# Kernel optimization log

Hardware: AMD Instinct MI355X
Metric: run time of the kernel (lower is better)

The kernel has to match this reference:

```python
import jax, jax.numpy as jnp
import numpy as np

DIM = 1024
HEADS = 16
HEAD_DIM = 64
INNER = HEADS * HEAD_DIM
SCALE = HEAD_DIM ** -0.5


def setup_inputs() -> dict:
    key = jax.random.key(0)
    k1, k2, k3, k4 = jax.random.split(key, 4)
    x = jax.random.normal(k1, (4, 2048, DIM), dtype=jnp.float32)
    # nn.Linear(dim, 3*inner) without bias; weight stored [out, in], we keep [in, out]
    w_qkv = jax.random.normal(k2, (DIM, 3 * INNER), dtype=jnp.float32) * (DIM ** -0.5)
    w_proj = jax.random.normal(k3, (INNER, DIM), dtype=jnp.float32) * (INNER ** -0.5)
    b_proj = jax.random.normal(k4, (DIM,), dtype=jnp.float32) * 0.01
    return {"x": x, "w_qkv": w_qkv, "w_proj": w_proj, "b_proj": b_proj}


def reference(x, w_qkv, w_proj, b_proj):
    B, N, _ = x.shape
    qkv = x @ w_qkv                                   # [B,N,3*inner]
    qkv = qkv.reshape(B, N, 3, HEADS, HEAD_DIM)
    q = qkv[:, :, 0].transpose(0, 2, 1, 3)           # [B,H,N,D]
    k = qkv[:, :, 1].transpose(0, 2, 1, 3)
    v = qkv[:, :, 2].transpose(0, 2, 1, 3)
    attn = jnp.einsum("bhqd,bhkd->bhqk", q, k) * SCALE
    attn = jax.nn.softmax(attn, axis=-1)
    out = jnp.einsum("bhqk,bhkd->bhqd", attn, v)     # [B,H,N,D]
    out = out.transpose(0, 2, 1, 3).reshape(B, N, INNER)
    return out @ w_proj + b_proj
```

## Files before the change

kernel.cpp:

```cpp
#include <hip/hip_runtime.h>

typedef unsigned short u16;
typedef unsigned int   u32;
typedef __attribute__((ext_vector_type(2))) float    f32x2;
typedef __attribute__((ext_vector_type(4))) float    f32x4;
typedef __attribute__((ext_vector_type(8))) __bf16   bf16x8;
typedef __attribute__((ext_vector_type(8))) unsigned short u16x8;
typedef __attribute__((ext_vector_type(4))) unsigned short u16x4;
typedef __attribute__((ext_vector_type(4))) float    float4v;

#define MFMA16(a,b,c) __builtin_amdgcn_mfma_f32_16x16x32_bf16((a),(b),(c),0,0,0)
#define QSCALE 0.18033688011112042f

__device__ __forceinline__ u16 f2b(float f){
  union { float f; unsigned u; } v; v.f = f;
  return (u16)((v.u + 0x7fffu + ((v.u >> 16) & 1u)) >> 16);
}

__device__ __forceinline__ u32 cvt_pk_bf16(float lo, float hi){
  u32 r;
  asm("v_cvt_pk_bf16_f32 %0, %1, %2" : "=v"(r) : "v"(lo), "v"(hi));
  return r;
}

__device__ __forceinline__ float exp2_raw(float x){
  float r;
  asm("v_exp_f32 %0, %1" : "=v"(r) : "v"(x));
  return r;
}

__device__ __forceinline__ f32x2 lo2(f32x4 v){ return __builtin_shufflevector(v, v, 0, 1); }
__device__ __forceinline__ f32x2 hi2(f32x4 v){ return __builtin_shufflevector(v, v, 2, 3); }

__device__ __forceinline__ void gload_lds16(const void* g, void* l){
  __builtin_amdgcn_global_load_lds(
      (const __attribute__((address_space(1))) void*)g,
      (__attribute__((address_space(3))) void*)l, 16, 0, 0);
}

__global__ void cast_f32_bf16(const float* __restrict__ in, u16* __restrict__ out, int n4){
  int i = blockIdx.x * blockDim.x + threadIdx.x;
  int st = gridDim.x * blockDim.x;
  for (; i < n4; i += st){
    float4v v = ((const float4v*)in)[i];
    u16x4 o;
    o[0] = f2b(v[0]); o[1] = f2b(v[1]); o[2] = f2b(v[2]); o[3] = f2b(v[3]);
    ((u16x4*)out)[i] = o;
  }
}

__global__ void tcast(const float* __restrict__ src, u16* __restrict__ dst, int R, int C){
  __shared__ float tile[32][33];
  int tx = threadIdx.x, ty = threadIdx.y;
  int c0 = blockIdx.x * 32, r0 = blockIdx.y * 32;
  #pragma unroll
  for (int i = 0; i < 4; i++)
    tile[ty + i*8][tx] = src[(long)(r0 + ty + i*8) * C + c0 + tx];
  __syncthreads();
  #pragma unroll
  for (int i = 0; i < 4; i++)
    dst[(long)(c0 + ty + i*8) * R + r0 + tx] = f2b(tile[tx][ty + i*8]);
}

template<int MODE>
__global__ __launch_bounds__(512, 2) void gemm8(
    const u16* __restrict__ A, const u16* __restrict__ Bt,
    int M, int N, int K,
    float* __restrict__ outF, const float* __restrict__ bias,
    u16* __restrict__ qb, u16* __restrict__ kb, u16* __restrict__ vtb)
{
  extern __shared__ u16 lds[];
  u16* aL = lds;
  u16* bL = lds + 49152;

  const int t  = threadIdx.x;
  const int l  = t & 63, lr = l & 15, lg = l >> 4;
  const int w  = t >> 6;
  const int wm = w >> 2, wn = (w >> 1) & 1, wk = w & 1;
  const int bid = blockIdx.x;
  const int xcd = bid & 7, idx = bid >> 3;
  const long mbase = (long)(xcd*4 + (idx & 3)) * 256;
  const long nbase = (long)(idx >> 2) * 128;

  const int xr0 = t >> 3;
  const int xc  = t & 7;
  const int xswz = (xc ^ (xr0 & 7)) << 3;

#define STG(F_) do { \
    const int T_ = (F_) >> 2, h_ = (F_) & 3, slot_ = T_ % 3; \
    if ((h_ & 1) == 0){ const int ah = h_ >> 1; \
      const u16* g_ = A + (mbase + ah*128 + xr0)*(long)K + T_*64 + xswz; \
      u16* d_ = aL + slot_*16384 + ah*8192 + t*8; \
      gload_lds16(g_, d_); \
      gload_lds16(g_ + 64*(long)K, d_ + 4096); \
    } else { const int bh_ = h_ >> 1; \
      const u16* g_ = Bt + (nbase + bh_*64 + xr0)*(long)K + T_*64 + xswz; \
      gload_lds16(g_, bL + slot_*8192 + bh_*4096 + t*8); } \
  } while(0)

#define VMCNT(n) asm volatile("s_waitcnt vmcnt(" #n ")" ::: "memory")
#define BAR() __builtin_amdgcn_s_barrier()

  f32x4 z = {0.f,0.f,0.f,0.f};
  f32x4 acc[8][4];
  #pragma unroll
  for (int a = 0; a < 8; a++)
    #pragma unroll
    for (int j = 0; j < 4; j++) acc[a][j] = z;

  const int kc = wk*4;

  STG(0); STG(1); STG(2); STG(3);
  STG(4); STG(5); STG(6); STG(7);
  VMCNT(6);
  BAR();

  for (int T = 0; T < 16; ++T){
    const int abuf = (T % 3) * 16384;
    const int bbuf = (T % 3) * 8192;
    bf16x8 afi[8], bfj[4];

    #pragma unroll
    for (int j = 0; j < 4; j++){
      const int rb = wn*64 + j*16 + lr;
      bfj[j] = *(const bf16x8*)&bL[bbuf + rb*64 + (((kc+lg)^(rb&7))<<3)];
    }
    #pragma unroll
    for (int i = 0; i < 8; i++){
      const int ra = wm*128 + i*16 + lr;
      afi[i] = *(const bf16x8*)&aL[abuf + ra*64 + (((kc+lg)^(ra&7))<<3)];
    }
    if (T < 14){
      STG(4*(T+2)); STG(4*(T+2)+1); STG(4*(T+2)+2); STG(4*(T+2)+3);
      VMCNT(6);
    } else if (T == 14){
      VMCNT(0);
    }
    BAR();
    __builtin_amdgcn_s_setprio(1);
    #pragma unroll
    for (int i = 0; i < 8; i++)
      #pragma unroll
      for (int j = 0; j < 4; j++)
        acc[i][j] = MFMA16(afi[i], bfj[j], acc[i][j]);
    __builtin_amdgcn_s_setprio(0);
    BAR();
  }
#undef STG
#undef VMCNT
#undef BAR

  if (wk){
    #pragma unroll
    for (int a = 0; a < 8; a++){
      f32x4 t0 = acc[a][0]; acc[a][0] = acc[a][2]; acc[a][2] = t0;
      f32x4 t1 = acc[a][1]; acc[a][1] = acc[a][3]; acc[a][3] = t1;
    }
  }
  f32x4* red = (f32x4*)lds;
  const int pb = (wm*2 + wn)*2;
  const int wme = pb + (1 - wk);
  const int rme = pb + wk;
  #pragma unroll
  for (int a = 0; a < 8; a++){
    red[(wme*2 + 0)*64 + l] = acc[a][2];
    red[(wme*2 + 1)*64 + l] = acc[a][3];
    __builtin_amdgcn_s_barrier();
    acc[a][0] += red[(rme*2 + 0)*64 + l];
    acc[a][1] += red[(rme*2 + 1)*64 + l];
    __builtin_amdgcn_s_barrier();
  }

  if (MODE == 0){
    #pragma unroll
    for (int a = 0; a < 8; a++){
      #pragma unroll
      for (int jj = 0; jj < 2; jj++){
        int col   = (int)nbase + wn*64 + (wk*2 + jj)*16 + lr;
        int which = col >> 10;
        int h     = (col >> 6) & 15;
        int d     = col & 63;
        int m0    = (int)mbase + wm*128 + a*16 + lg*4;
        int b     = m0 >> 11, ns0 = m0 & 2047;
        int bh    = (b << 4) + h;
        f32x4 v   = (jj == 0) ? acc[a][0] : acc[a][1];
        if (which == 2){
          u16x4 pk;
          #pragma unroll
          for (int r = 0; r < 4; r++) pk[r] = f2b(v[r]);
          *(u16x4*)&vtb[((long)bh*64 + d)*2048 + ns0] = pk;
        } else {
          u16* dst  = (which == 0) ? qb : kb;
          float scl = (which == 0) ? QSCALE : 1.0f;
          #pragma unroll
          for (int r = 0; r < 4; r++)
            dst[((long)bh * 2048 + ns0 + r) * 64 + d] = f2b(v[r] * scl);
        }
      }
    }
  } else {
    #pragma unroll
    for (int a = 0; a < 8; a++){
      #pragma unroll
      for (int jj = 0; jj < 2; jj++){
        int c = (int)nbase + wn*64 + (wk*2 + jj)*16 + lr;
        float bv = bias[c];
        f32x4 v = (jj == 0) ? acc[a][0] : acc[a][1];
        #pragma unroll
        for (int r = 0; r < 4; r++){
          int m = (int)mbase + wm*128 + a*16 + lg*4 + r;
          outF[(long)m * N + c] = v[r] + bv;
        }
      }
    }
  }
}

__global__ __launch_bounds__(256, 2) void attn_fused(
    const u16* __restrict__ qb, const u16* __restrict__ kb,
    const u16* __restrict__ vtb, u16* __restrict__ ob)
{
  __shared__ u16 k_lds[2][64*64];
  __shared__ u16 vt_lds[2][64*64];
  const int t  = threadIdx.x;
  const int l  = t & 63, lr = l & 15, lg = l >> 4;
  const int w  = t >> 6;
  const int bid = blockIdx.x;
  const int vid = (bid & 7) * 64 + (bid >> 3);
  const int bh = vid >> 3, qt = vid & 7;
  const int qrow = qt*256 + w*64;
  const int h7 = lr & 7;

  const u16* Qp = qb + ((long)bh*2048 + qrow)*64;
  bf16x8 qf0[4], qf1[4];
  #pragma unroll
  for (int g = 0; g < 4; g++){
    qf0[g] = *(const bf16x8*)&Qp[(g*16+lr)*64 + lg*8];
    qf1[g] = *(const bf16x8*)&Qp[(g*16+lr)*64 + 32 + lg*8];
  }

  const int r1 = t >> 3;
  const int cx = ((t & 7) ^ (r1 & 7)) * 8;
  const u16* Kp = kb  + (long)bh*2048*64;
  const u16* Vt = vtb + (long)bh*64*2048;
  const int koff0 = r1*64 + cx,        koff1 = (r1+32)*64 + cx;
  const int voff0 = r1*2048 + cx,      voff1 = (r1+32)*2048 + cx;

#define STAGE(kv, buf) do { \
    gload_lds16(Kp + (long)(kv)*64 + koff0, &k_lds[buf][t*8]); \
    gload_lds16(Kp + (long)(kv)*64 + koff1, &k_lds[buf][2048 + t*8]); \
    gload_lds16(Vt + (kv) + voff0, &vt_lds[buf][t*8]); \
    gload_lds16(Vt + (kv) + voff1, &vt_lds[buf][2048 + t*8]); \
  } while(0)

  f32x4 z = {0.f,0.f,0.f,0.f};
  f32x4 oacc[4][4];
  f32x2 sacc[4];
  #pragma unroll
  for (int g = 0; g < 4; g++){
    sacc[g] = (f32x2){0.f, 0.f};
    #pragma unroll
    for (int nt = 0; nt < 4; nt++) oacc[g][nt] = z;
  }

  STAGE(0, 0);
  for (int it = 0; it < 32; ++it){
    const int cur = it & 1;
    __syncthreads();
    if (it < 31) STAGE((it+1)*64, cur^1);

    const u16* kl = k_lds[cur];
    const u16* vl = vt_lds[cur];

    f32x4 st[4][4];
    __builtin_amdgcn_s_setprio(1);
    #pragma unroll
    for (int k4 = 0; k4 < 4; k4++){
      const int row = (k4*16 + lr)*64;
      bf16x8 kf0 = *(const bf16x8*)&kl[row + ((0+lg)^h7)*8];
      bf16x8 kf1 = *(const bf16x8*)&kl[row + ((4+lg)^h7)*8];
      #pragma unroll
      for (int g = 0; g < 4; g++){
        st[g][k4] = MFMA16(kf0, qf0[g], z);
        st[g][k4] = MFMA16(kf1, qf1[g], st[g][k4]);
      }
    }
    __builtin_amdgcn_s_setprio(0);

    bf16x8 pa0[4], pa1[4];
    #pragma unroll
    for (int g = 0; g < 4; g++){
      u32 wv[4][2];
      #pragma unroll
      for (int k4 = 0; k4 < 4; k4++){
        f32x2 e0 = lo2(st[g][k4]), e1 = hi2(st[g][k4]);
        e0[0] = exp2_raw(e0[0]); e0[1] = exp2_raw(e0[1]);
        e1[0] = exp2_raw(e1[0]); e1[1] = exp2_raw(e1[1]);
        sacc[g] += e0 + e1;
        wv[k4][0] = cvt_pk_bf16(e0[0], e0[1]);
        wv[k4][1] = cvt_pk_bf16(e1[0], e1[1]);
      }
      union { u32 u[4]; bf16x8 v; } p0, p1;
      p0.u[0]=wv[0][0]; p0.u[1]=wv[0][1]; p0.u[2]=wv[1][0]; p0.u[3]=wv[1][1];
      p1.u[0]=wv[2][0]; p1.u[1]=wv[2][1]; p1.u[2]=wv[3][0]; p1.u[3]=wv[3][1];
      pa0[g] = p0.v; pa1[g] = p1.v;
    }

    const int vhalf = (lg & 1) * 4;
    const int cA    = lg >> 1;
    #pragma unroll
    for (int nt = 0; nt < 4; nt++){
      const int rb = (nt*16 + lr)*64;
      u16x4 a0_ = *(const u16x4*)&vl[rb + ((cA     ^ h7)*8) + vhalf];
      u16x4 a1_ = *(const u16x4*)&vl[rb + (((cA+2) ^ h7)*8) + vhalf];
      u16x4 a2_ = *(const u16x4*)&vl[rb + (((cA+4) ^ h7)*8) + vhalf];
      u16x4 a3_ = *(const u16x4*)&vl[rb + (((cA+6) ^ h7)*8) + vhalf];
      u16x8 s0 = __builtin_shufflevector(a0_, a1_, 0,1,2,3,4,5,6,7);
      u16x8 s1 = __builtin_shufflevector(a2_, a3_, 0,1,2,3,4,5,6,7);
      __builtin_amdgcn_s_setprio(1);
      #pragma unroll
      for (int g = 0; g < 4; g++){
        oacc[g][nt] = MFMA16(pa0[g], *(bf16x8*)&s0, oacc[g][nt]);
        oacc[g][nt] = MFMA16(pa1[g], *(bf16x8*)&s1, oacc[g][nt]);
      }
      __builtin_amdgcn_s_setprio(0);
    }
  }
#undef STAGE

  const int b = bh >> 4, h = bh & 15;
  #pragma unroll
  for (int g = 0; g < 4; g++){
    float rs = sacc[g][0] + sacc[g][1];
    rs += __shfl_xor(rs, 16, 64);
    rs += __shfl_xor(rs, 32, 64);
    float linv = 1.0f / rs;
    #pragma unroll
    for (int r = 0; r < 4; r++){
      float lrr = __shfl(linv, lg*4 + r, 64);
      long m = (long)b*2048 + qrow + g*16 + lg*4 + r;
      #pragma unroll
      for (int nt = 0; nt < 4; nt++)
        ob[m*1024 + h*64 + nt*16 + lr] = f2b(oacc[g][nt][r] * lrr);
    }
  }
}

extern "C" void kernel_launch(void* const* d_in, const int* in_sizes, int n_in,
                              void* d_out, int out_size, void* d_ws, size_t ws_size,
                              hipStream_t stream)
{
  const float* x      = (const float*)d_in[0];
  const float* w_qkv  = (const float*)d_in[1];
  const float* w_proj = (const float*)d_in[2];
  const float* b_proj = (const float*)d_in[3];
  float* out = (float*)d_out;

  char* ws = (char*)d_ws;
  size_t off = 0;
  u16* xb     = (u16*)(ws + off);
  u16* obuf   = xb;
  off += (size_t)8192*1024*2;
  u16* wqkvt  = (u16*)(ws + off); off += (size_t)3072*1024*2;
  u16* wprojt = (u16*)(ws + off); off += (size_t)1024*1024*2;
  u16* qbuf   = (u16*)(ws + off); off += (size_t)64*2048*64*2;
  u16* kbuf   = (u16*)(ws + off); off += (size_t)64*2048*64*2;
  u16* vtb    = (u16*)(ws + off); off += (size_t)64*64*2048*2;

  hipFuncSetAttribute(reinterpret_cast<const void*>(&gemm8<0>),
                      hipFuncAttributeMaxDynamicSharedMemorySize, 147456);
  hipFuncSetAttribute(reinterpret_cast<const void*>(&gemm8<1>),
                      hipFuncAttributeMaxDynamicSharedMemorySize, 147456);

  cast_f32_bf16<<<2048, 256, 0, stream>>>(x, xb, (8192*1024)/4);
  tcast<<<dim3(96, 32), dim3(32, 8), 0, stream>>>(w_qkv, wqkvt, 1024, 3072);
  tcast<<<dim3(32, 32), dim3(32, 8), 0, stream>>>(w_proj, wprojt, 1024, 1024);

  gemm8<0><<<dim3(768), 512, 147456, stream>>>(xb, wqkvt, 8192, 3072, 1024,
                                               nullptr, nullptr, qbuf, kbuf, vtb);
  attn_fused<<<dim3(512), 256, 0, stream>>>(qbuf, kbuf, vtb, obuf);
  gemm8<1><<<dim3(256), 512, 147456, stream>>>(obuf, wprojt, 8192, 1024, 1024,
                                               out, b_proj, nullptr, nullptr, nullptr);
}
```

Measured before the change: 181.0 us.

## Split attention KV range across two blocks and add a combine kernel

Each attention block now handles half of the key/value sequence, which doubles the grid from 512 to 1024 blocks. Each half writes unnormalized bf16 partial outputs and per-row sums of exponentials. A new combine kernel adds the two partials and divides by the total row sum before the output projection. The aim is more parallelism and better latency hiding on the CUs, at the cost of an extra kernel launch, extra global memory traffic for the partials, and an extra bf16 rounding step.

```diff
diff --git a/kernel.cpp b/kernel.cpp
--- a/kernel.cpp
+++ b/kernel.cpp
@@ -15,6 +15,11 @@
 __device__ __forceinline__ u16 f2b(float f){
   union { float f; unsigned u; } v; v.f = f;
   return (u16)((v.u + 0x7fffu + ((v.u >> 16) & 1u)) >> 16);
+}
+
+__device__ __forceinline__ float b2f(u16 u){
+  union { unsigned u; float f; } v; v.u = ((u32)u) << 16;
+  return v.f;
 }
 
 __device__ __forceinline__ u32 cvt_pk_bf16(float lo, float hi){
@@ -218,7 +223,8 @@
 
 __global__ __launch_bounds__(256, 2) void attn_fused(
     const u16* __restrict__ qb, const u16* __restrict__ kb,
-    const u16* __restrict__ vtb, u16* __restrict__ ob)
+    const u16* __restrict__ vtb,
+    u16* __restrict__ po0, u16* __restrict__ po1, float* __restrict__ ls)
 {
   __shared__ u16 k_lds[2][64*64];
   __shared__ u16 vt_lds[2][64*64];
@@ -226,10 +232,16 @@
   const int l  = t & 63, lr = l & 15, lg = l >> 4;
   const int w  = t >> 6;
   const int bid = blockIdx.x;
-  const int vid = (bid & 7) * 64 + (bid >> 3);
-  const int bh = vid >> 3, qt = vid & 7;
+  const int vid = (bid & 7) * 128 + (bid >> 3);
+  const int bh   = vid >> 4;
+  const int qt   = (vid >> 1) & 7;
+  const int half = vid & 1;
   const int qrow = qt*256 + w*64;
+  const int kvbase = half * 1024;
   const int h7 = lr & 7;
+
+  u16* pob = half ? po1 : po0;
+  float* lsb = ls + half * (64*2048);
 
   const u16* Qp = qb + ((long)bh*2048 + qrow)*64;
   bf16x8 qf0[4], qf1[4];
@@ -263,11 +275,11 @@
     for (int nt = 0; nt < 4; nt++) oacc[g][nt] = z;
   }
 
-  STAGE(0, 0);
-  for (int it = 0; it < 32; ++it){
+  STAGE(kvbase, 0);
+  for (int it = 0; it < 16; ++it){
     const int cur = it & 1;
     __syncthreads();
-    if (it < 31) STAGE((it+1)*64, cur^1);
+    if (it < 15) STAGE(kvbase + (it+1)*64, cur^1);
 
     const u16* kl = k_lds[cur];
     const u16* vl = vt_lds[cur];
@@ -334,15 +346,36 @@
     float rs = sacc[g][0] + sacc[g][1];
     rs += __shfl_xor(rs, 16, 64);
     rs += __shfl_xor(rs, 32, 64);
-    float linv = 1.0f / rs;
+    if (lg == 0) lsb[bh*2048 + qrow + g*16 + lr] = rs;
     #pragma unroll
     for (int r = 0; r < 4; r++){
-      float lrr = __shfl(linv, lg*4 + r, 64);
       long m = (long)b*2048 + qrow + g*16 + lg*4 + r;
       #pragma unroll
       for (int nt = 0; nt < 4; nt++)
-        ob[m*1024 + h*64 + nt*16 + lr] = f2b(oacc[g][nt][r] * lrr);
-    }
+        pob[m*1024 + h*64 + nt*16 + lr] = f2b(oacc[g][nt][r]);
+    }
+  }
+}
+
+__global__ void attn_combine(const u16* __restrict__ po0, const u16* __restrict__ po1,
+                             const float* __restrict__ ls, u16* __restrict__ ob)
+{
+  int gid = blockIdx.x * blockDim.x + threadIdx.x;
+  int st  = gridDim.x * blockDim.x;
+  for (; gid < 8192*128; gid += st){
+    int m  = gid >> 7;
+    int c8 = (gid & 127) * 8;
+    int h  = c8 >> 6;
+    int bh = ((m >> 11) << 4) + h;
+    int q  = m & 2047;
+    float inv = 1.0f / (ls[bh*2048 + q] + ls[64*2048 + bh*2048 + q]);
+    u16x8 a = *(const u16x8*)&po0[(long)m*1024 + c8];
+    u16x8 b = *(const u16x8*)&po1[(long)m*1024 + c8];
+    u16x8 o;
+    #pragma unroll
+    for (int j = 0; j < 8; j++)
+      o[j] = f2b((b2f(a[j]) + b2f(b[j])) * inv);
+    *(u16x8*)&ob[(long)m*1024 + c8] = o;
   }
 }
 
@@ -359,13 +392,16 @@
   char* ws = (char*)d_ws;
   size_t off = 0;
   u16* xb     = (u16*)(ws + off);
-  u16* obuf   = xb;
+  u16* po0    = xb;
   off += (size_t)8192*1024*2;
   u16* wqkvt  = (u16*)(ws + off); off += (size_t)3072*1024*2;
   u16* wprojt = (u16*)(ws + off); off += (size_t)1024*1024*2;
   u16* qbuf   = (u16*)(ws + off); off += (size_t)64*2048*64*2;
+  u16* obuf   = qbuf;
   u16* kbuf   = (u16*)(ws + off); off += (size_t)64*2048*64*2;
   u16* vtb    = (u16*)(ws + off); off += (size_t)64*64*2048*2;
+  u16* po1    = (u16*)(ws + off); off += (size_t)8192*1024*2;
+  float* ls   = (float*)(ws + off); off += (size_t)2*64*2048*4;
 
   hipFuncSetAttribute(reinterpret_cast<const void*>(&gemm8<0>),
                       hipFuncAttributeMaxDynamicSharedMemorySize, 147456);
@@ -378,7 +414,8 @@
 
   gemm8<0><<<dim3(768), 512, 147456, stream>>>(xb, wqkvt, 8192, 3072, 1024,
                                                nullptr, nullptr, qbuf, kbuf, vtb);
-  attn_fused<<<dim3(512), 256, 0, stream>>>(qbuf, kbuf, vtb, obuf);
+  attn_fused<<<dim3(1024), 256, 0, stream>>>(qbuf, kbuf, vtb, po0, po1, ls);
+  attn_combine<<<dim3(2048), 256, 0, stream>>>(po0, po1, ls, obuf);
   gemm8<1><<<dim3(256), 512, 147456, stream>>>(obuf, wprojt, 8192, 1024, 1024,
                                                out, b_proj, nullptr, nullptr, nullptr);
 }
```

After: 190.6 us. +5.3%, slower.
